# Kernel optimization log

Measured on AMD Instinct MI355X. Metric: run time of the kernel, lower is better.

The kernel has to match this reference:

```python
import jax, jax.numpy as jnp
import numpy as np

N_VOX = 100000   # active voxels
K = 27           # 3^3 kernel offsets
M = 60000        # matched (in, out) pairs per offset
CIN = 64
COUT = 64
BN_EPS = 1e-5


def setup_inputs() -> dict:
    key = jax.random.key(0)
    ks = jax.random.split(key, 6)
    feats = jax.random.normal(ks[0], (N_VOX, CIN), dtype=jnp.float32)
    W = jax.random.normal(ks[1], (K, CIN, COUT), dtype=jnp.float32) * 0.05
    gamma = jnp.ones((COUT,), dtype=jnp.float32)
    beta = jnp.zeros((COUT,), dtype=jnp.float32)
    running_mean = jax.random.normal(ks[2], (COUT,), dtype=jnp.float32) * 0.1
    running_var = jax.random.uniform(ks[3], (COUT,), dtype=jnp.float32, minval=0.5, maxval=1.5)
    in_idx = jax.random.randint(ks[4], (K, M), 0, N_VOX, dtype=jnp.int32)
    out_idx = jax.random.randint(ks[5], (K, M), 0, N_VOX, dtype=jnp.int32)
    return {
        "feats": feats, "W": W, "gamma": gamma, "beta": beta,
        "running_mean": running_mean, "running_var": running_var,
        "in_idx": in_idx, "out_idx": out_idx,
    }


def reference(feats, W, gamma, beta, running_mean, running_var, in_idx, out_idx):
    # Sparse conv as gather-GEMM-scatter over the hash-map kernel map.
    gathered = feats[in_idx]                              # [K, M, Cin]
    contrib = jnp.einsum('kmc,kcd->kmd', gathered, W)     # [K, M, Cout]
    out = jax.ops.segment_sum(
        contrib.reshape(-1, W.shape[-1]),                 # [K*M, Cout]
        out_idx.reshape(-1),
        num_segments=feats.shape[0],
    )                                                     # [N, Cout]
    # BatchNorm (inference, running stats) + ReLU
    inv = jax.lax.rsqrt(running_var + BN_EPS)
    y = (out - running_mean) * (inv * gamma) + beta
    return jnp.maximum(y, 0.0)
```

## Files before the change

### kernel.cpp

```cpp
#include <hip/hip_runtime.h>

#define N_VOX 100000
#define K_OFF 27
#define M_PAIR 60000
#define NPAIR (K_OFF * M_PAIR)
#define CIN 64
#define COUT 64
#define BN_EPS 1e-5f

#define VB_SHIFT 8
#define VB (1 << VB_SHIFT)
#define NB ((N_VOX + VB - 1) / VB)
#define BCAP 5120
#define PPT 16
#define PA_PAIRS (256 * PPT)
#define PA_GRID ((NPAIR + PA_PAIRS - 1) / PA_PAIRS)

#define TILES_PER_WAVE 10
#define WAVES_PER_K (M_PAIR / 16 / TILES_PER_WAVE)
#define CONV_BLOCKS_X ((WAVES_PER_K + 3) / 4)

typedef __attribute__((ext_vector_type(8))) short bf16x8;
typedef __attribute__((ext_vector_type(8))) unsigned short u16x8;
typedef __attribute__((ext_vector_type(4))) unsigned int u32x4;
typedef __attribute__((ext_vector_type(2))) int i32x2;
typedef __attribute__((ext_vector_type(4))) float f32x4;

__device__ __forceinline__ unsigned short f32_to_bf16(float f) {
    unsigned int u = __float_as_uint(f);
    u += 0x7FFFu + ((u >> 16) & 1u);
    return (unsigned short)(u >> 16);
}
__device__ __forceinline__ float bf16_lo(unsigned int u) {
    return __uint_as_float(u << 16);
}
__device__ __forceinline__ float bf16_hi(unsigned int u) {
    return __uint_as_float(u & 0xffff0000u);
}

__global__ __launch_bounds__(256) void scatter_pairs_kernel(
    const int* __restrict__ oix,
    unsigned int* __restrict__ recs, int* __restrict__ bucketCount,
    const float* __restrict__ feats, unsigned short* __restrict__ fb,
    const float* __restrict__ W, unsigned short* __restrict__ Wt,
    const float* __restrict__ gamma, const float* __restrict__ beta,
    const float* __restrict__ rmean, const float* __restrict__ rvar,
    float* __restrict__ bnscale, float* __restrict__ bnshift)
{
    __shared__ int lhist[NB];
    __shared__ int gbase[NB];
    const int t = threadIdx.x;
    for (int i = t; i < NB; i += 256) lhist[i] = 0;
    __syncthreads();

    const int base = blockIdx.x * PA_PAIRS;
    int vsave[PPT];
    int lpos[PPT];
#pragma unroll
    for (int i = 0; i < PPT; ++i) {
        const int e = base + i * 256 + t;
        int v = -1, lp = 0;
        if (e < NPAIR) {
            v = oix[e];
            lp = atomicAdd(&lhist[v >> VB_SHIFT], 1);
        }
        vsave[i] = v;
        lpos[i] = lp;
    }
    __syncthreads();
    for (int i = t; i < NB; i += 256) {
        const int c = lhist[i];
        gbase[i] = c ? atomicAdd(&bucketCount[i], c) : 0;
    }
    __syncthreads();
#pragma unroll
    for (int i = 0; i < PPT; ++i) {
        const int v = vsave[i];
        if (v >= 0) {
            const int e = base + i * 256 + t;
            const int b = v >> VB_SHIFT;
            const int idx = gbase[b] + lpos[i];
            if (idx < BCAP)
                recs[(size_t)b * BCAP + idx] =
                    ((unsigned int)e << VB_SHIFT) | (unsigned int)(v & (VB - 1));
        }
    }

    const int gid = blockIdx.x * 256 + t;
    const int nt = PA_GRID * 256;
    for (int e4i = gid; e4i < (N_VOX * CIN) / 4; e4i += nt) {
        const int e4 = e4i * 4;
        const float4 v = *(const float4*)(feats + e4);
        ushort4 b;
        b.x = f32_to_bf16(v.x);
        b.y = f32_to_bf16(v.y);
        b.z = f32_to_bf16(v.z);
        b.w = f32_to_bf16(v.w);
        *(ushort4*)(fb + e4) = b;
    }
    for (int e = gid; e < K_OFF * CIN * COUT; e += nt) {
        const int k = e / (CIN * COUT);
        const int r = e % (CIN * COUT);
        Wt[k * CIN * COUT + (r % COUT) * CIN + (r / COUT)] = f32_to_bf16(W[e]);
    }
    if (gid < COUT) {
        const float inv = rsqrtf(rvar[gid] + BN_EPS);
        const float sc = inv * gamma[gid];
        bnscale[gid] = sc;
        bnshift[gid] = beta[gid] - rmean[gid] * sc;
    }
}

__global__ __launch_bounds__(512) void bucket_scan_kernel(
    const int* __restrict__ bucketCount, int* __restrict__ bucketBase)
{
    __shared__ int part[512];
    const int t = threadIdx.x;
    int c = 0;
    if (t < NB) {
        c = bucketCount[t];
        if (c > BCAP) c = BCAP;
    }
    part[t] = c;
    __syncthreads();
    for (int o = 1; o < 512; o <<= 1) {
        int x = (t >= o) ? part[t - o] : 0;
        __syncthreads();
        part[t] += x;
        __syncthreads();
    }
    if (t < NB) bucketBase[t] = part[t] - c;
}

__global__ __launch_bounds__(256) void perm_seg_kernel(
    const unsigned int* __restrict__ recs, const int* __restrict__ bucketCount,
    const int* __restrict__ bucketBase,
    int* __restrict__ perm, i32x2* __restrict__ segcnt)
{
    __shared__ int hist[VB];
    __shared__ int part[VB];
    const int b = blockIdx.x;
    const int t = threadIdx.x;
    hist[t] = 0;
    __syncthreads();
    int bc = bucketCount[b];
    if (bc > BCAP) bc = BCAP;
    const unsigned int* r = recs + (size_t)b * BCAP;
    for (int i = t; i < bc; i += 256)
        atomicAdd(&hist[r[i] & (VB - 1)], 1);
    __syncthreads();
    const int c = hist[t];
    part[t] = c;
    __syncthreads();
    for (int o = 1; o < 256; o <<= 1) {
        int x = (t >= o) ? part[t - o] : 0;
        __syncthreads();
        part[t] += x;
        __syncthreads();
    }
    const int gbase = bucketBase[b];
    const int excl = part[t] - c;
    const int v = b * VB + t;
    if (v < N_VOX) {
        i32x2 sc;
        sc.x = gbase + excl;
        sc.y = c;
        segcnt[v] = sc;
    }
    __syncthreads();
    hist[t] = excl;
    __syncthreads();
    for (int i = t; i < bc; i += 256) {
        const unsigned int rec = r[i];
        const int lp = atomicAdd(&hist[rec & (VB - 1)], 1);
        perm[gbase + lp] = (int)(rec >> VB_SHIFT);
    }
}

__global__ __launch_bounds__(256) void conv_kernel(
    const unsigned short* __restrict__ fb, const unsigned short* __restrict__ Wt,
    const int* __restrict__ in_idx,
    unsigned short* __restrict__ contrib)
{
    __shared__ alignas(16) unsigned short lds[4][16 * 72];
    const int k = blockIdx.y;
    const int lane = threadIdx.x & 63;
    const int wid = threadIdx.x >> 6;
    const int w = blockIdx.x * 4 + wid;
    if (w >= WAVES_PER_K) return;
    const int col = lane & 15;
    const int quad = lane >> 4;
    unsigned short* L = lds[wid];

    bf16x8 Bf[4][2];
    const short* Wk = (const short*)(Wt + k * CIN * COUT);
#pragma unroll
    for (int t = 0; t < 4; ++t) {
        const short* p = Wk + (t * 16 + col) * CIN + quad * 8;
        Bf[t][0] = *(const bf16x8*)(p);
        Bf[t][1] = *(const bf16x8*)(p + 32);
    }

    int m0 = k * M_PAIR + (w * TILES_PER_WAVE) * 16;
    {
        const int rin = in_idx[m0 + col];
        const short* fp = (const short*)fb + (size_t)rin * CIN + quad * 8;
        bf16x8 A0 = *(const bf16x8*)(fp);
        bf16x8 A1 = *(const bf16x8*)(fp + 32);

        for (int it = 0; it < TILES_PER_WAVE; ++it) {
            bf16x8 nA0 = A0, nA1 = A1;
            if (it + 1 < TILES_PER_WAVE) {
                const int rn = in_idx[m0 + 16 + col];
                const short* fn = (const short*)fb + (size_t)rn * CIN + quad * 8;
                nA0 = *(const bf16x8*)(fn);
                nA1 = *(const bf16x8*)(fn + 32);
            }

            f32x4 acc[4];
#pragma unroll
            for (int t = 0; t < 4; ++t) {
                f32x4 z = {0.f, 0.f, 0.f, 0.f};
                acc[t] = __builtin_amdgcn_mfma_f32_16x16x32_bf16(A0, Bf[t][0], z, 0, 0, 0);
                acc[t] = __builtin_amdgcn_mfma_f32_16x16x32_bf16(A1, Bf[t][1], acc[t], 0, 0, 0);
            }
#pragma unroll
            for (int r = 0; r < 4; ++r) {
                const int row = quad * 4 + r;
#pragma unroll
                for (int t = 0; t < 4; ++t)
                    L[row * 72 + t * 16 + col] = f32_to_bf16(acc[t][r]);
            }
#pragma unroll
            for (int itr = 0; itr < 2; ++itr) {
                const int row = itr * 8 + (lane >> 3);
                const int chunk = lane & 7;
                const u16x8 v = *(const u16x8*)(L + row * 72 + chunk * 8);
                *(u16x8*)(contrib + (size_t)(m0 + row) * 64 + chunk * 8) = v;
            }
            A0 = nA0;
            A1 = nA1;
            m0 += 16;
        }
    }
}

__global__ __launch_bounds__(256) void gather_bn_kernel(
    const unsigned short* __restrict__ contrib, const int* __restrict__ perm,
    const i32x2* __restrict__ segcnt,
    const float* __restrict__ bnscale, const float* __restrict__ bnshift,
    float* __restrict__ out)
{
    const int v = blockIdx.x * 4 + (threadIdx.x >> 6);
    if (v >= N_VOX) return;
    const int lane = threadIdx.x & 63;
    const int rg = lane >> 3;
    const int cg = lane & 7;
    const i32x2 sc = segcnt[v];
    const int s = sc.x;
    const int n = sc.y;

    float a0 = 0.f, a1 = 0.f, a2 = 0.f, a3 = 0.f;
    float a4 = 0.f, a5 = 0.f, a6 = 0.f, a7 = 0.f;
    float b0 = 0.f, b1 = 0.f, b2 = 0.f, b3 = 0.f;
    float b4 = 0.f, b5 = 0.f, b6 = 0.f, b7 = 0.f;
    int j = rg;
    for (; j + 8 < n; j += 16) {
        const int p0 = perm[s + j];
        const int p1 = perm[s + j + 8];
        const u32x4 u = __builtin_nontemporal_load(
            (const u32x4*)(contrib + (size_t)p0 * 64) + cg);
        const u32x4 w = __builtin_nontemporal_load(
            (const u32x4*)(contrib + (size_t)p1 * 64) + cg);
        a0 += bf16_lo(u.x); a1 += bf16_hi(u.x);
        a2 += bf16_lo(u.y); a3 += bf16_hi(u.y);
        a4 += bf16_lo(u.z); a5 += bf16_hi(u.z);
        a6 += bf16_lo(u.w); a7 += bf16_hi(u.w);
        b0 += bf16_lo(w.x); b1 += bf16_hi(w.x);
        b2 += bf16_lo(w.y); b3 += bf16_hi(w.y);
        b4 += bf16_lo(w.z); b5 += bf16_hi(w.z);
        b6 += bf16_lo(w.w); b7 += bf16_hi(w.w);
    }
    for (; j < n; j += 8) {
        const int p0 = perm[s + j];
        const u32x4 u = __builtin_nontemporal_load(
            (const u32x4*)(contrib + (size_t)p0 * 64) + cg);
        a0 += bf16_lo(u.x); a1 += bf16_hi(u.x);
        a2 += bf16_lo(u.y); a3 += bf16_hi(u.y);
        a4 += bf16_lo(u.z); a5 += bf16_hi(u.z);
        a6 += bf16_lo(u.w); a7 += bf16_hi(u.w);
    }
    a0 += b0; a1 += b1; a2 += b2; a3 += b3;
    a4 += b4; a5 += b5; a6 += b6; a7 += b7;
    a0 += __shfl_xor(a0, 8, 64); a0 += __shfl_xor(a0, 16, 64); a0 += __shfl_xor(a0, 32, 64);
    a1 += __shfl_xor(a1, 8, 64); a1 += __shfl_xor(a1, 16, 64); a1 += __shfl_xor(a1, 32, 64);
    a2 += __shfl_xor(a2, 8, 64); a2 += __shfl_xor(a2, 16, 64); a2 += __shfl_xor(a2, 32, 64);
    a3 += __shfl_xor(a3, 8, 64); a3 += __shfl_xor(a3, 16, 64); a3 += __shfl_xor(a3, 32, 64);
    a4 += __shfl_xor(a4, 8, 64); a4 += __shfl_xor(a4, 16, 64); a4 += __shfl_xor(a4, 32, 64);
    a5 += __shfl_xor(a5, 8, 64); a5 += __shfl_xor(a5, 16, 64); a5 += __shfl_xor(a5, 32, 64);
    a6 += __shfl_xor(a6, 8, 64); a6 += __shfl_xor(a6, 16, 64); a6 += __shfl_xor(a6, 32, 64);
    a7 += __shfl_xor(a7, 8, 64); a7 += __shfl_xor(a7, 16, 64); a7 += __shfl_xor(a7, 32, 64);
    if (rg == 0) {
        const int ch = cg * 8;
        float4 r0, r1;
        r0.x = fmaxf(fmaf(a0, bnscale[ch + 0], bnshift[ch + 0]), 0.f);
        r0.y = fmaxf(fmaf(a1, bnscale[ch + 1], bnshift[ch + 1]), 0.f);
        r0.z = fmaxf(fmaf(a2, bnscale[ch + 2], bnshift[ch + 2]), 0.f);
        r0.w = fmaxf(fmaf(a3, bnscale[ch + 3], bnshift[ch + 3]), 0.f);
        r1.x = fmaxf(fmaf(a4, bnscale[ch + 4], bnshift[ch + 4]), 0.f);
        r1.y = fmaxf(fmaf(a5, bnscale[ch + 5], bnshift[ch + 5]), 0.f);
        r1.z = fmaxf(fmaf(a6, bnscale[ch + 6], bnshift[ch + 6]), 0.f);
        r1.w = fmaxf(fmaf(a7, bnscale[ch + 7], bnshift[ch + 7]), 0.f);
        *(float4*)(out + (size_t)v * 64 + ch) = r0;
        *(float4*)(out + (size_t)v * 64 + ch + 4) = r1;
    }
}

__global__ __launch_bounds__(256) void prep_small_kernel(
    const float* __restrict__ feats, unsigned short* __restrict__ fb,
    float* __restrict__ out, const float* __restrict__ W,
    unsigned short* __restrict__ Wt)
{
    const int e = blockIdx.x * blockDim.x + threadIdx.x;
    if (e < (N_VOX * CIN) / 4) {
        const int e4 = e * 4;
        const float4 v = *(const float4*)(feats + e4);
        ushort4 b;
        b.x = f32_to_bf16(v.x);
        b.y = f32_to_bf16(v.y);
        b.z = f32_to_bf16(v.z);
        b.w = f32_to_bf16(v.w);
        *(ushort4*)(fb + e4) = b;
        *(float4*)(out + e4) = make_float4(0.f, 0.f, 0.f, 0.f);
    }
    if (e < K_OFF * CIN * COUT) {
        const int k = e / (CIN * COUT);
        const int r = e % (CIN * COUT);
        Wt[k * CIN * COUT + (r % COUT) * CIN + (r / COUT)] = f32_to_bf16(W[e]);
    }
}

__global__ __launch_bounds__(256) void conv_atomic_kernel(
    const unsigned short* __restrict__ fb, const unsigned short* __restrict__ Wt,
    const int* __restrict__ in_idx, const int* __restrict__ out_idx,
    float* __restrict__ out)
{
    const int k = blockIdx.y;
    const int lane = threadIdx.x & 63;
    const int wave = blockIdx.x * 4 + (threadIdx.x >> 6);
    const int col = lane & 15;
    const int quad = lane >> 4;
    bf16x8 Bf[4][2];
    const short* Wk = (const short*)(Wt + k * CIN * COUT);
#pragma unroll
    for (int t = 0; t < 4; ++t) {
        const short* p = Wk + (t * 16 + col) * CIN + quad * 8;
        Bf[t][0] = *(const bf16x8*)(p);
        Bf[t][1] = *(const bf16x8*)(p + 32);
    }
    const int base = k * M_PAIR;
    for (int tile = wave; tile < M_PAIR / 16; tile += 128) {
        const int m0 = base + tile * 16;
        const int rin = in_idx[m0 + col];
        const short* fp = (const short*)fb + (size_t)rin * CIN + quad * 8;
        const bf16x8 A0 = *(const bf16x8*)(fp);
        const bf16x8 A1 = *(const bf16x8*)(fp + 32);
        f32x4 acc[4];
#pragma unroll
        for (int t = 0; t < 4; ++t) {
            f32x4 z = {0.f, 0.f, 0.f, 0.f};
            acc[t] = __builtin_amdgcn_mfma_f32_16x16x32_bf16(A0, Bf[t][0], z, 0, 0, 0);
            acc[t] = __builtin_amdgcn_mfma_f32_16x16x32_bf16(A1, Bf[t][1], acc[t], 0, 0, 0);
        }
        int vo[4];
#pragma unroll
        for (int r = 0; r < 4; ++r) vo[r] = out_idx[m0 + quad * 4 + r];
#pragma unroll
        for (int r = 0; r < 4; ++r) {
            float* op = out + (size_t)vo[r] * COUT + col;
#pragma unroll
            for (int t = 0; t < 4; ++t) atomicAdd(op + t * 16, acc[t][r]);
        }
    }
}

__global__ __launch_bounds__(256) void bn_relu_kernel(
    float* __restrict__ out,
    const float* __restrict__ gamma, const float* __restrict__ beta,
    const float* __restrict__ mean, const float* __restrict__ var)
{
    const int e = blockIdx.x * blockDim.x + threadIdx.x;
    if (e >= N_VOX * COUT) return;
    const int c = e & (COUT - 1);
    const float inv = rsqrtf(var[c] + BN_EPS);
    const float y = (out[e] - mean[c]) * (inv * gamma[c]) + beta[c];
    out[e] = fmaxf(y, 0.f);
}

extern "C" void kernel_launch(void* const* d_in, const int* in_sizes, int n_in,
                              void* d_out, int out_size, void* d_ws, size_t ws_size,
                              hipStream_t stream) {
    const float* feats = (const float*)d_in[0];
    const float* W     = (const float*)d_in[1];
    const float* gamma = (const float*)d_in[2];
    const float* beta  = (const float*)d_in[3];
    const float* rmean = (const float*)d_in[4];
    const float* rvar  = (const float*)d_in[5];
    const int* in_idx  = (const int*)d_in[6];
    const int* out_idx = (const int*)d_in[7];
    float* out = (float*)d_out;

    char* ws = (char*)d_ws;
    size_t off = 0;
    auto alloc = [&](size_t bytes) {
        size_t p = off;
        off = (off + bytes + 255) & ~(size_t)255;
        return p;
    };
    const size_t o_fb   = alloc((size_t)N_VOX * CIN * 2);
    const size_t o_wt   = alloc((size_t)K_OFF * CIN * COUT * 2);
    const size_t o_bc   = alloc((size_t)NB * 4);
    const size_t o_bb   = alloc((size_t)NB * 4);
    const size_t o_recs = alloc((size_t)NB * BCAP * 4);
    const size_t o_sc   = alloc((size_t)N_VOX * 8);
    const size_t o_bn   = alloc((size_t)2 * COUT * 4);
    const size_t o_perm = alloc((size_t)NPAIR * 4);
    const size_t o_ctr  = alloc((size_t)NPAIR * COUT * 2);
    const bool big = (ws_size >= off);

    unsigned short* fb  = (unsigned short*)(ws + o_fb);
    unsigned short* Wt  = (unsigned short*)(ws + o_wt);
    int* bucketCount    = (int*)(ws + o_bc);
    int* bucketBase     = (int*)(ws + o_bb);
    unsigned int* recs  = (unsigned int*)(ws + o_recs);
    i32x2* segcnt       = (i32x2*)(ws + o_sc);
    float* bnscale      = (float*)(ws + o_bn);
    float* bnshift      = bnscale + COUT;
    int* perm           = (int*)(ws + o_perm);
    unsigned short* ctr = (unsigned short*)(ws + o_ctr);

    if (big) {
        hipError_t _e = hipMemsetAsync(bucketCount, 0, (size_t)NB * 4, stream);
        (void)_e;
        scatter_pairs_kernel<<<PA_GRID, 256, 0, stream>>>(
            out_idx, recs, bucketCount, feats, fb, W, Wt,
            gamma, beta, rmean, rvar, bnscale, bnshift);
        bucket_scan_kernel<<<1, 512, 0, stream>>>(bucketCount, bucketBase);
        perm_seg_kernel<<<NB, 256, 0, stream>>>(recs, bucketCount, bucketBase,
                                                perm, segcnt);
        conv_kernel<<<dim3(CONV_BLOCKS_X, K_OFF), 256, 0, stream>>>(
            fb, Wt, in_idx, ctr);
        gather_bn_kernel<<<(N_VOX + 3) / 4, 256, 0, stream>>>(
            ctr, perm, segcnt, bnscale, bnshift, out);
    } else {
        const int ptot = (N_VOX * CIN) / 4;
        prep_small_kernel<<<(ptot + 255) / 256, 256, 0, stream>>>(feats, fb, out, W, Wt);
        conv_atomic_kernel<<<dim3(32, K_OFF), 256, 0, stream>>>(fb, Wt, in_idx, out_idx, out);
        const int total_e = N_VOX * COUT;
        bn_relu_kernel<<<(total_e + 255) / 256, 256, 0, stream>>>(out, gamma, beta, rmean, rvar);
    }
}
```

Baseline: 251.3 us.

## Fuse bucket scatter into conv kernel and scan into perm kernel

Moves the out_idx bucketing histogram and scatter work into the conv kernel's blocks, so it overlaps with the gather-GEMM instead of running as a separate pass. The single-block bucket scan is folded into perm_seg_kernel: every block redundantly rescans the bucket counts. The memset is replaced by zeroing inside the prep kernel. Together these cut the launch count from six operations to four. In exchange, the conv blocks take on extra LDS and a serial bucketing phase, and each perm block repeats the same scan.

```diff
diff --git a/kernel.cpp b/kernel.cpp
--- a/kernel.cpp
+++ b/kernel.cpp
@@ -38,56 +38,16 @@
     return __uint_as_float(u & 0xffff0000u);
 }
 
-__global__ __launch_bounds__(256) void scatter_pairs_kernel(
-    const int* __restrict__ oix,
-    unsigned int* __restrict__ recs, int* __restrict__ bucketCount,
+__global__ __launch_bounds__(256) void prep_kernel(
     const float* __restrict__ feats, unsigned short* __restrict__ fb,
     const float* __restrict__ W, unsigned short* __restrict__ Wt,
     const float* __restrict__ gamma, const float* __restrict__ beta,
     const float* __restrict__ rmean, const float* __restrict__ rvar,
-    float* __restrict__ bnscale, float* __restrict__ bnshift)
-{
-    __shared__ int lhist[NB];
-    __shared__ int gbase[NB];
-    const int t = threadIdx.x;
-    for (int i = t; i < NB; i += 256) lhist[i] = 0;
-    __syncthreads();
-
-    const int base = blockIdx.x * PA_PAIRS;
-    int vsave[PPT];
-    int lpos[PPT];
-#pragma unroll
-    for (int i = 0; i < PPT; ++i) {
-        const int e = base + i * 256 + t;
-        int v = -1, lp = 0;
-        if (e < NPAIR) {
-            v = oix[e];
-            lp = atomicAdd(&lhist[v >> VB_SHIFT], 1);
-        }
-        vsave[i] = v;
-        lpos[i] = lp;
-    }
-    __syncthreads();
-    for (int i = t; i < NB; i += 256) {
-        const int c = lhist[i];
-        gbase[i] = c ? atomicAdd(&bucketCount[i], c) : 0;
-    }
-    __syncthreads();
-#pragma unroll
-    for (int i = 0; i < PPT; ++i) {
-        const int v = vsave[i];
-        if (v >= 0) {
-            const int e = base + i * 256 + t;
-            const int b = v >> VB_SHIFT;
-            const int idx = gbase[b] + lpos[i];
-            if (idx < BCAP)
-                recs[(size_t)b * BCAP + idx] =
-                    ((unsigned int)e << VB_SHIFT) | (unsigned int)(v & (VB - 1));
-        }
-    }
-
-    const int gid = blockIdx.x * 256 + t;
-    const int nt = PA_GRID * 256;
+    float* __restrict__ bnscale, float* __restrict__ bnshift,
+    int* __restrict__ bucketCount)
+{
+    const int gid = blockIdx.x * 256 + threadIdx.x;
+    const int nt = gridDim.x * 256;
     for (int e4i = gid; e4i < (N_VOX * CIN) / 4; e4i += nt) {
         const int e4 = e4i * 4;
         const float4 v = *(const float4*)(feats + e4);
@@ -109,81 +69,52 @@
         bnscale[gid] = sc;
         bnshift[gid] = beta[gid] - rmean[gid] * sc;
     }
-}
-
-__global__ __launch_bounds__(512) void bucket_scan_kernel(
-    const int* __restrict__ bucketCount, int* __restrict__ bucketBase)
-{
-    __shared__ int part[512];
+    if (gid < NB) bucketCount[gid] = 0;
+}
+
+__global__ __launch_bounds__(256) void conv_bucket_kernel(
+    const unsigned short* __restrict__ fb, const unsigned short* __restrict__ Wt,
+    const int* __restrict__ in_idx, const int* __restrict__ oix,
+    unsigned int* __restrict__ recs, int* __restrict__ bucketCount,
+    unsigned short* __restrict__ contrib)
+{
+    __shared__ alignas(16) unsigned short lds[4][16 * 72];
+    __shared__ int lhist[NB];
+    __shared__ int gbase[NB];
     const int t = threadIdx.x;
-    int c = 0;
-    if (t < NB) {
-        c = bucketCount[t];
-        if (c > BCAP) c = BCAP;
-    }
-    part[t] = c;
-    __syncthreads();
-    for (int o = 1; o < 512; o <<= 1) {
-        int x = (t >= o) ? part[t - o] : 0;
-        __syncthreads();
-        part[t] += x;
-        __syncthreads();
-    }
-    if (t < NB) bucketBase[t] = part[t] - c;
-}
-
-__global__ __launch_bounds__(256) void perm_seg_kernel(
-    const unsigned int* __restrict__ recs, const int* __restrict__ bucketCount,
-    const int* __restrict__ bucketBase,
-    int* __restrict__ perm, i32x2* __restrict__ segcnt)
-{
-    __shared__ int hist[VB];
-    __shared__ int part[VB];
-    const int b = blockIdx.x;
-    const int t = threadIdx.x;
-    hist[t] = 0;
-    __syncthreads();
-    int bc = bucketCount[b];
-    if (bc > BCAP) bc = BCAP;
-    const unsigned int* r = recs + (size_t)b * BCAP;
-    for (int i = t; i < bc; i += 256)
-        atomicAdd(&hist[r[i] & (VB - 1)], 1);
-    __syncthreads();
-    const int c = hist[t];
-    part[t] = c;
-    __syncthreads();
-    for (int o = 1; o < 256; o <<= 1) {
-        int x = (t >= o) ? part[t - o] : 0;
-        __syncthreads();
-        part[t] += x;
-        __syncthreads();
-    }
-    const int gbase = bucketBase[b];
-    const int excl = part[t] - c;
-    const int v = b * VB + t;
-    if (v < N_VOX) {
-        i32x2 sc;
-        sc.x = gbase + excl;
-        sc.y = c;
-        segcnt[v] = sc;
-    }
-    __syncthreads();
-    hist[t] = excl;
-    __syncthreads();
-    for (int i = t; i < bc; i += 256) {
-        const unsigned int rec = r[i];
-        const int lp = atomicAdd(&hist[rec & (VB - 1)], 1);
-        perm[gbase + lp] = (int)(rec >> VB_SHIFT);
-    }
-}
-
-__global__ __launch_bounds__(256) void conv_kernel(
-    const unsigned short* __restrict__ fb, const unsigned short* __restrict__ Wt,
-    const int* __restrict__ in_idx,
-    unsigned short* __restrict__ contrib)
-{
-    __shared__ alignas(16) unsigned short lds[4][16 * 72];
     const int k = blockIdx.y;
+    const int fid = k * CONV_BLOCKS_X + blockIdx.x;
+
+    if (fid < PA_GRID) {
+        for (int i = t; i < NB; i += 256) lhist[i] = 0;
+        __syncthreads();
+        const int base = fid * PA_PAIRS;
+        int lp[PPT];
+#pragma unroll
+        for (int i = 0; i < PPT; ++i) {
+            const int e = base + i * 256 + t;
+            lp[i] = (e < NPAIR) ? atomicAdd(&lhist[oix[e] >> VB_SHIFT], 1) : 0;
+        }
+        __syncthreads();
+        for (int i = t; i < NB; i += 256) {
+            const int c = lhist[i];
+            gbase[i] = c ? atomicAdd(&bucketCount[i], c) : 0;
+        }
+        __syncthreads();
+#pragma unroll
+        for (int i = 0; i < PPT; ++i) {
+            const int e = base + i * 256 + t;
+            if (e < NPAIR) {
+                const int v = oix[e];
+                const int b = v >> VB_SHIFT;
+                const int idx = gbase[b] + lp[i];
+                if (idx < BCAP)
+                    recs[(size_t)b * BCAP + idx] =
+                        ((unsigned int)e << VB_SHIFT) | (unsigned int)(v & (VB - 1));
+            }
+        }
+    }
+
     const int lane = threadIdx.x & 63;
     const int wid = threadIdx.x >> 6;
     const int w = blockIdx.x * 4 + wid;
@@ -195,10 +126,10 @@
     bf16x8 Bf[4][2];
     const short* Wk = (const short*)(Wt + k * CIN * COUT);
 #pragma unroll
-    for (int t = 0; t < 4; ++t) {
-        const short* p = Wk + (t * 16 + col) * CIN + quad * 8;
-        Bf[t][0] = *(const bf16x8*)(p);
-        Bf[t][1] = *(const bf16x8*)(p + 32);
+    for (int tt = 0; tt < 4; ++tt) {
+        const short* p = Wk + (tt * 16 + col) * CIN + quad * 8;
+        Bf[tt][0] = *(const bf16x8*)(p);
+        Bf[tt][1] = *(const bf16x8*)(p + 32);
     }
 
     int m0 = k * M_PAIR + (w * TILES_PER_WAVE) * 16;
@@ -219,17 +150,17 @@
 
             f32x4 acc[4];
 #pragma unroll
-            for (int t = 0; t < 4; ++t) {
+            for (int tt = 0; tt < 4; ++tt) {
                 f32x4 z = {0.f, 0.f, 0.f, 0.f};
-                acc[t] = __builtin_amdgcn_mfma_f32_16x16x32_bf16(A0, Bf[t][0], z, 0, 0, 0);
-                acc[t] = __builtin_amdgcn_mfma_f32_16x16x32_bf16(A1, Bf[t][1], acc[t], 0, 0, 0);
+                acc[tt] = __builtin_amdgcn_mfma_f32_16x16x32_bf16(A0, Bf[tt][0], z, 0, 0, 0);
+                acc[tt] = __builtin_amdgcn_mfma_f32_16x16x32_bf16(A1, Bf[tt][1], acc[tt], 0, 0, 0);
             }
 #pragma unroll
             for (int r = 0; r < 4; ++r) {
                 const int row = quad * 4 + r;
 #pragma unroll
-                for (int t = 0; t < 4; ++t)
-                    L[row * 72 + t * 16 + col] = f32_to_bf16(acc[t][r]);
+                for (int tt = 0; tt < 4; ++tt)
+                    L[row * 72 + tt * 16 + col] = f32_to_bf16(acc[tt][r]);
             }
 #pragma unroll
             for (int itr = 0; itr < 2; ++itr) {
@@ -242,6 +173,71 @@
             A1 = nA1;
             m0 += 16;
         }
+    }
+}
+
+__global__ __launch_bounds__(512) void perm_seg_kernel(
+    const unsigned int* __restrict__ recs, const int* __restrict__ bucketCount,
+    int* __restrict__ perm, i32x2* __restrict__ segcnt)
+{
+    __shared__ int scan[512];
+    __shared__ int hist[VB];
+    __shared__ int gb_sh, bc_sh;
+    const int b = blockIdx.x;
+    const int t = threadIdx.x;
+    int c = 0;
+    if (t < NB) {
+        c = bucketCount[t];
+        if (c > BCAP) c = BCAP;
+    }
+    scan[t] = c;
+    __syncthreads();
+    for (int o = 1; o < 512; o <<= 1) {
+        int x = (t >= o) ? scan[t - o] : 0;
+        __syncthreads();
+        scan[t] += x;
+        __syncthreads();
+    }
+    if (t == b) {
+        gb_sh = scan[t] - c;
+        bc_sh = c;
+    }
+    if (t < VB) hist[t] = 0;
+    __syncthreads();
+    const int bc = bc_sh;
+    const int gbase = gb_sh;
+    const unsigned int* r = recs + (size_t)b * BCAP;
+    for (int i = t; i < bc; i += 512)
+        atomicAdd(&hist[r[i] & (VB - 1)], 1);
+    __syncthreads();
+    int hc = 0;
+    if (t < VB) {
+        hc = hist[t];
+        scan[t] = hc;
+    }
+    __syncthreads();
+    for (int o = 1; o < VB; o <<= 1) {
+        int x = (t < VB && t >= o) ? scan[t - o] : 0;
+        __syncthreads();
+        if (t < VB) scan[t] += x;
+        __syncthreads();
+    }
+    if (t < VB) {
+        const int excl = scan[t] - hc;
+        const int v = b * VB + t;
+        if (v < N_VOX) {
+            i32x2 sc2;
+            sc2.x = gbase + excl;
+            sc2.y = hc;
+            segcnt[v] = sc2;
+        }
+        hist[t] = excl;
+    }
+    __syncthreads();
+    for (int i = t; i < bc; i += 512) {
+        const unsigned int rec = r[i];
+        const int lp = atomicAdd(&hist[rec & (VB - 1)], 1);
+        perm[gbase + lp] = (int)(rec >> VB_SHIFT);
     }
 }
 
@@ -420,7 +416,6 @@
     const size_t o_fb   = alloc((size_t)N_VOX * CIN * 2);
     const size_t o_wt   = alloc((size_t)K_OFF * CIN * COUT * 2);
     const size_t o_bc   = alloc((size_t)NB * 4);
-    const size_t o_bb   = alloc((size_t)NB * 4);
     const size_t o_recs = alloc((size_t)NB * BCAP * 4);
     const size_t o_sc   = alloc((size_t)N_VOX * 8);
     const size_t o_bn   = alloc((size_t)2 * COUT * 4);
@@ -431,7 +426,6 @@
     unsigned short* fb  = (unsigned short*)(ws + o_fb);
     unsigned short* Wt  = (unsigned short*)(ws + o_wt);
     int* bucketCount    = (int*)(ws + o_bc);
-    int* bucketBase     = (int*)(ws + o_bb);
     unsigned int* recs  = (unsigned int*)(ws + o_recs);
     i32x2* segcnt       = (i32x2*)(ws + o_sc);
     float* bnscale      = (float*)(ws + o_bn);
@@ -440,16 +434,12 @@
     unsigned short* ctr = (unsigned short*)(ws + o_ctr);
 
     if (big) {
-        hipError_t _e = hipMemsetAsync(bucketCount, 0, (size_t)NB * 4, stream);
-        (void)_e;
-        scatter_pairs_kernel<<<PA_GRID, 256, 0, stream>>>(
-            out_idx, recs, bucketCount, feats, fb, W, Wt,
-            gamma, beta, rmean, rvar, bnscale, bnshift);
-        bucket_scan_kernel<<<1, 512, 0, stream>>>(bucketCount, bucketBase);
-        perm_seg_kernel<<<NB, 256, 0, stream>>>(recs, bucketCount, bucketBase,
-                                                perm, segcnt);
-        conv_kernel<<<dim3(CONV_BLOCKS_X, K_OFF), 256, 0, stream>>>(
-            fb, Wt, in_idx, ctr);
+        prep_kernel<<<2048, 256, 0, stream>>>(
+            feats, fb, W, Wt, gamma, beta, rmean, rvar,
+            bnscale, bnshift, bucketCount);
+        conv_bucket_kernel<<<dim3(CONV_BLOCKS_X, K_OFF), 256, 0, stream>>>(
+            fb, Wt, in_idx, out_idx, recs, bucketCount, ctr);
+        perm_seg_kernel<<<NB, 512, 0, stream>>>(recs, bucketCount, perm, segcnt);
         gather_bn_kernel<<<(N_VOX + 3) / 4, 256, 0, stream>>>(
             ctr, perm, segcnt, bnscale, bnshift, out);
     } else {
```

Result: faster. 228.0 us (-9.3%).
